# Kernel optimization log

Hardware: AMD Instinct MI355X
Metric: run time of the kernel (lower is better)

## Reference

```python
import jax, jax.numpy as jnp
import numpy as np

B, S, D, H, RANK, NC = 2, 2048, 1024, 16, 128, 16
DH = D // H


def setup_inputs() -> dict:
    key = jax.random.key(0)
    ks = jax.random.split(key, 10)
    x = jax.random.normal(ks[0], (B, S, D), jnp.float32)
    # causal mask, broadcast over batch and heads like torch's [B,1,S,S]
    mask = jnp.tril(jnp.ones((S, S), dtype=bool))[None, None]
    # orthogonal-ish init approximated by scaled gaussian
    compress_neurons = jax.random.normal(ks[1], (NC, D, RANK), jnp.float32) / np.sqrt(D)
    router_Q = jax.random.normal(ks[2], (NC, D), jnp.float32) * 0.02
    router_K = jax.random.normal(ks[3], (NC, D), jnp.float32) * 0.02
    router_V = jax.random.normal(ks[4], (NC, D), jnp.float32) * 0.02
    wQ = jax.random.normal(ks[5], (D, RANK), jnp.float32) / np.sqrt(RANK)
    wK = jax.random.normal(ks[6], (D, RANK), jnp.float32) / np.sqrt(RANK)
    wV = jax.random.normal(ks[7], (D, RANK), jnp.float32) / np.sqrt(RANK)
    wO = jax.random.normal(ks[8], (D, D), jnp.float32) / np.sqrt(D)
    return {"x": x, "mask": mask, "compress_neurons": compress_neurons,
            "router_Q": router_Q, "router_K": router_K, "router_V": router_V,
            "wQ": wQ, "wK": wK, "wV": wV, "wO": wO}


def reference(x, mask, compress_neurons, router_Q, router_K, router_V, wQ, wK, wV, wO):
    def compress(router_w):
        # router scores -> softmax over all n_compress neurons
        w = jax.nn.softmax(jnp.einsum('bsd,nd->bsn', x, router_w), axis=-1)  # [B,S,NC]
        # softmax-weighted sum of all neuron projections (fused einsum)
        return jnp.einsum('bsd,ndr,bsn->bsr', x, compress_neurons, w)  # [B,S,RANK]

    hQ = compress(router_Q)
    hK = compress(router_K)
    hV = compress(router_V)
    # expand rank -> d_model (Linear weight [D,RANK]), then split heads
    Q = jnp.einsum('bsr,dr->bsd', hQ, wQ).reshape(B, S, H, DH).transpose(0, 2, 1, 3)
    K = jnp.einsum('bsr,dr->bsd', hK, wK).reshape(B, S, H, DH).transpose(0, 2, 1, 3)
    V = jnp.einsum('bsr,dr->bsd', hV, wV).reshape(B, S, H, DH).transpose(0, 2, 1, 3)
    scores = jnp.einsum('bhqd,bhkd->bhqk', Q, K) / np.sqrt(DH)  # [B,H,S,S]
    scores = jnp.where(mask, scores, -jnp.inf)
    attn = jax.nn.softmax(scores, axis=-1)
    attn_out = jnp.einsum('bhqk,bhkd->bhqd', attn, V)
    attn_out = attn_out.transpose(0, 2, 1, 3).reshape(B, S, D)
    # dropout omitted (eval mode / dropout=0)
    return jnp.einsum('bsd,ed->bse', attn_out, wO)
```

## Files before the change

### kernel.cpp

```cpp
#include <hip/hip_runtime.h>
#include <hip/hip_bf16.h>
#include <math.h>

#define B_ 2
#define S_ 2048
#define D_ 1024
#define H_ 16
#define RANK_ 128
#define NC_ 16
#define DH_ 64
#define T_ (B_*S_)
#define NZ_ 2176
#define ZW_ 2048

typedef __attribute__((ext_vector_type(8))) __bf16 bf16x8;
typedef __attribute__((ext_vector_type(8))) unsigned short u16x8;
typedef __attribute__((ext_vector_type(4))) unsigned short u16x4;
typedef __attribute__((ext_vector_type(4))) float f32x4;
typedef __attribute__((ext_vector_type(16))) float f32x16;

#if __has_builtin(__builtin_amdgcn_exp2f)
#define EXP2F(x) __builtin_amdgcn_exp2f(x)
#else
#define EXP2F(x) exp2f(x)
#endif

__device__ __forceinline__ unsigned short f2bu(float f) {
    __hip_bfloat16 h = __float2bfloat16(f);
    unsigned short u; __builtin_memcpy(&u, &h, 2); return u;
}
__device__ __forceinline__ float bu2f(unsigned short u) {
    __hip_bfloat16 h; __builtin_memcpy(&h, &u, 2); return __bfloat162float(h);
}

__device__ __forceinline__ void gl_lds16(const unsigned short* g, unsigned short* l) {
    __builtin_amdgcn_global_load_lds(
        (const __attribute__((address_space(1))) void*)g,
        (__attribute__((address_space(3))) void*)l, 16, 0, 0);
}

__device__ __forceinline__ unsigned cvtpk_bf16(float lo, float hi) {
    unsigned r;
    asm("v_cvt_pk_bf16_f32 %0, %1, %2" : "=v"(r) : "v"(lo), "v"(hi));
    return r;
}
__device__ __forceinline__ void plswap(unsigned &a, unsigned &b) {
    asm("v_permlane32_swap_b32 %0, %1" : "+v"(a), "+v"(b));
}

__device__ __forceinline__ bool sniff_f32(const unsigned* __restrict__ p) {
    int votes = 0;
    #pragma unroll
    for (int i = 0; i < 64; i++) {
        unsigned e = (p[i] >> 23) & 0xFFu;
        votes += (e >= 0x60u && e <= 0x8Fu) ? 1 : 0;
    }
    return votes >= 32;
}

struct Cvt { const void* src[9]; unsigned short* dst[9]; const void* C; unsigned short* Ct; };

__global__ __launch_bounds__(256) void k_inputs(Cvt cv,
    const unsigned* __restrict__ probe)
{
    bool f32 = sniff_f32(probe);
    if (blockIdx.x < 512) {
        int bid = blockIdx.x;
        int d0 = (bid & 15) * 64, r0 = ((bid >> 4) & 1) * 64, n = bid >> 5;
        __shared__ unsigned short tile[64][65];
        for (int idx = threadIdx.x; idx < 4096; idx += 256) {
            int row = idx >> 6, col = idx & 63;
            size_t si = ((size_t)n*D_ + d0 + row)*RANK_ + r0 + col;
            tile[row][col] = f32 ? f2bu(((const float*)cv.C)[si])
                                 : ((const unsigned short*)cv.C)[si];
        }
        __syncthreads();
        for (int idx = threadIdx.x; idx < 4096; idx += 256) {
            int row = idx >> 6, col = idx & 63;
            cv.Ct[((size_t)(n*RANK_ + r0 + row))*D_ + d0 + col] = tile[col][row];
        }
        return;
    }
    const int offs[9] = {0, 4194304, 4210688, 4227072, 4243456,
                         4259840, 4390912, 4521984, 4653056};
    const int total4 = 5701632 / 4;
    int nconv = gridDim.x - 512;
    int stride = nconv * 256;
    for (int g = (blockIdx.x - 512) * 256 + threadIdx.x; g < total4; g += stride) {
        int i = g * 4;
        int seg = 0;
        #pragma unroll
        for (int s = 1; s < 9; s++) seg += (i >= offs[s]) ? 1 : 0;
        int local = i - offs[seg];
        const void* sp = cv.src[seg];
        u16x4 v = {0, 0, 0, 0};
        if (sp) {
            if (f32) {
                f32x4 x = *(const f32x4*)((const float*)sp + local);
                #pragma unroll
                for (int j = 0; j < 4; j++) v[j] = f2bu(x[j]);
            } else {
                v = *(const u16x4*)((const unsigned short*)sp + local);
            }
        }
        *(u16x4*)(cv.dst[seg] + local) = v;
    }
}

template<int MT, int MODE>
__global__ __launch_bounds__(256) void k_mfma_gemm(const unsigned short* __restrict__ A,
    const unsigned short* __restrict__ Bm, void* __restrict__ Cout,
    const unsigned* __restrict__ probe, int M, int N, int K)
{
    bool f32out = false;
    if (MODE == 2) f32out = sniff_f32(probe);
    __shared__ __align__(16) unsigned short As[MT*32*32];
    __shared__ __align__(16) unsigned short Bs[128*32];
    const int tid = threadIdx.x;
    const int wv = tid >> 6, lane = tid & 63;
    const int wm = (wv >> 1) * (MT*16), wn = (wv & 1) * 64;
    const int quad = lane >> 4, l16 = lane & 15;
    const int m0 = blockIdx.x * (MT*32), n0 = blockIdx.y * 128;

    const f32x4 z4 = {0.f, 0.f, 0.f, 0.f};
    f32x4 acc[MT][4];
    #pragma unroll
    for (int i = 0; i < MT; i++)
        #pragma unroll
        for (int j = 0; j < 4; j++) acc[i][j] = z4;

    for (int k0 = 0; k0 < K; k0 += 32) {
        __syncthreads();
        #pragma unroll
        for (int c = 0; c < MT/2; c++) {
            int idx = wv*64 + c*256 + lane;
            gl_lds16(A + (size_t)(m0 + (idx >> 2))*K + k0 + (idx & 3)*8,
                     &As[(wv*64 + c*256)*8]);
        }
        #pragma unroll
        for (int c = 0; c < 2; c++) {
            int idx = wv*64 + c*256 + lane;
            gl_lds16(Bm + (size_t)(n0 + (idx >> 2))*K + k0 + (idx & 3)*8,
                     &Bs[(wv*64 + c*256)*8]);
        }
        __syncthreads();
        bf16x8 af[MT], bfr[4];
        #pragma unroll
        for (int mt = 0; mt < MT; mt++) af[mt]  = *(const bf16x8*)&As[(wm + mt*16 + l16)*32 + quad*8];
        #pragma unroll
        for (int nt = 0; nt < 4; nt++) bfr[nt] = *(const bf16x8*)&Bs[(wn + nt*16 + l16)*32 + quad*8];
        #pragma unroll
        for (int mt = 0; mt < MT; mt++)
            #pragma unroll
            for (int nt = 0; nt < 4; nt++)
                acc[mt][nt] = __builtin_amdgcn_mfma_f32_16x16x32_bf16(af[mt], bfr[nt], acc[mt][nt], 0, 0, 0);
    }
    #pragma unroll
    for (int mt = 0; mt < MT; mt++)
        #pragma unroll
        for (int nt = 0; nt < 4; nt++) {
            int col = n0 + wn + nt*16 + l16;
            #pragma unroll
            for (int r = 0; r < 4; r++) {
                int rowg = m0 + wm + mt*16 + quad*4 + r;
                float v = acc[mt][nt][r];
                if (MODE == 2 && f32out) ((float*)Cout)[(size_t)rowg*N + col] = v;
                else  ((unsigned short*)Cout)[(size_t)rowg*N + col] = f2bu(v);
            }
        }
}

__global__ __launch_bounds__(256) void k_zscore(const unsigned short* __restrict__ xc,
    const unsigned short* __restrict__ Ct, unsigned short* __restrict__ z,
    const unsigned short* __restrict__ Rt, float* __restrict__ spart)
{
    __shared__ __align__(16) unsigned short As[128*32];
    __shared__ __align__(16) unsigned short Bs[128*32];
    const int tid = threadIdx.x;
    const int wv = tid >> 6, lane = tid & 63;
    const int quad = lane >> 4, l16 = lane & 15;
    const f32x4 z4 = {0.f, 0.f, 0.f, 0.f};

    if (blockIdx.x < 512) {
        const int wm = (wv >> 1) * 64, wn = (wv & 1) * 64;
        const int m0 = (blockIdx.x & 31) * 128, n0 = (blockIdx.x >> 5) * 128;
        f32x4 acc[4][4];
        #pragma unroll
        for (int i = 0; i < 4; i++)
            #pragma unroll
            for (int j = 0; j < 4; j++) acc[i][j] = z4;

        for (int k0 = 0; k0 < D_; k0 += 32) {
            __syncthreads();
            #pragma unroll
            for (int c = 0; c < 2; c++) {
                int idx = wv*64 + c*256 + lane;
                gl_lds16(xc + (size_t)(m0 + (idx >> 2))*D_ + k0 + (idx & 3)*8,
                         &As[(wv*64 + c*256)*8]);
                gl_lds16(Ct + (size_t)(n0 + (idx >> 2))*D_ + k0 + (idx & 3)*8,
                         &Bs[(wv*64 + c*256)*8]);
            }
            __syncthreads();
            bf16x8 af[4], bfr[4];
            #pragma unroll
            for (int mt = 0; mt < 4; mt++) af[mt]  = *(const bf16x8*)&As[(wm + mt*16 + l16)*32 + quad*8];
            #pragma unroll
            for (int nt = 0; nt < 4; nt++) bfr[nt] = *(const bf16x8*)&Bs[(wn + nt*16 + l16)*32 + quad*8];
            #pragma unroll
            for (int mt = 0; mt < 4; mt++)
                #pragma unroll
                for (int nt = 0; nt < 4; nt++)
                    acc[mt][nt] = __builtin_amdgcn_mfma_f32_16x16x32_bf16(af[mt], bfr[nt], acc[mt][nt], 0, 0, 0);
        }
        #pragma unroll
        for (int mt = 0; mt < 4; mt++)
            #pragma unroll
            for (int nt = 0; nt < 4; nt++) {
                int col = n0 + wn + nt*16 + l16;
                #pragma unroll
                for (int r = 0; r < 4; r++) {
                    int rowg = m0 + wm + mt*16 + quad*4 + r;
                    z[(size_t)rowg*ZW_ + col] = f2bu(acc[mt][nt][r]);
                }
            }
    } else {
        const int id = blockIdx.x - 512;
        const int m0 = (id & 31) * 128;
        const int kc = id >> 5;
        const int wm = wv * 32;
        f32x4 acc[2][4];
        #pragma unroll
        for (int i = 0; i < 2; i++)
            #pragma unroll
            for (int j = 0; j < 4; j++) acc[i][j] = z4;

        for (int k0 = kc*128; k0 < kc*128 + 128; k0 += 32) {
            __syncthreads();
            #pragma unroll
            for (int c = 0; c < 2; c++) {
                int idx = wv*64 + c*256 + lane;
                gl_lds16(xc + (size_t)(m0 + (idx >> 2))*D_ + k0 + (idx & 3)*8,
                         &As[(wv*64 + c*256)*8]);
            }
            {
                int idx = wv*64 + lane;
                gl_lds16(Rt + (size_t)(idx >> 2)*D_ + k0 + (idx & 3)*8,
                         &Bs[(wv*64)*8]);
            }
            __syncthreads();
            bf16x8 af[2], bfr[4];
            #pragma unroll
            for (int mt = 0; mt < 2; mt++) af[mt]  = *(const bf16x8*)&As[(wm + mt*16 + l16)*32 + quad*8];
            #pragma unroll
            for (int nt = 0; nt < 4; nt++) bfr[nt] = *(const bf16x8*)&Bs[(nt*16 + l16)*32 + quad*8];
            #pragma unroll
            for (int mt = 0; mt < 2; mt++)
                #pragma unroll
                for (int nt = 0; nt < 4; nt++)
                    acc[mt][nt] = __builtin_amdgcn_mfma_f32_16x16x32_bf16(af[mt], bfr[nt], acc[mt][nt], 0, 0, 0);
        }
        #pragma unroll
        for (int mt = 0; mt < 2; mt++)
            #pragma unroll
            for (int nt = 0; nt < 4; nt++) {
                int col = nt*16 + l16;
                #pragma unroll
                for (int r = 0; r < 4; r++) {
                    int rowg = m0 + wm + mt*16 + quad*4 + r;
                    spart[(size_t)kc*T_*64 + (size_t)rowg*64 + col] = acc[mt][nt][r];
                }
            }
    }
}

__global__ __launch_bounds__(256) void k_hreduce(const unsigned short* __restrict__ z,
    const float* __restrict__ spart, unsigned short* __restrict__ h)
{
    int t0 = blockIdx.x * 2;
    int tg = threadIdx.x >> 7, r = threadIdx.x & 127;
    int t = t0 + tg;
    __shared__ float sc[2][48];
    __shared__ float wl[2][3][16];
    if (threadIdx.x < 96) {
        int tk = threadIdx.x / 48, j = threadIdx.x % 48;
        float s = 0.f;
        #pragma unroll
        for (int p = 0; p < 8; p++)
            s += spart[(size_t)p*T_*64 + (size_t)(t0 + tk)*64 + j];
        sc[tk][j] = s;
    }
    __syncthreads();
    if (threadIdx.x < 6) {
        int tk = threadIdx.x / 3, w = threadIdx.x % 3;
        float m = -INFINITY;
        for (int n = 0; n < 16; n++) m = fmaxf(m, sc[tk][w*16 + n]);
        float s = 0.f, e[16];
        for (int n = 0; n < 16; n++) { e[n] = __expf(sc[tk][w*16 + n] - m); s += e[n]; }
        float inv = 1.f / s;
        for (int n = 0; n < 16; n++) wl[tk][w][n] = e[n] * inv;
    }
    __syncthreads();
    const unsigned short* zr = z + (size_t)t * ZW_;
    float acc[3] = {0.f, 0.f, 0.f};
    #pragma unroll
    for (int n = 0; n < NC_; n++) {
        float zv = bu2f(zr[n*RANK_ + r]);
        #pragma unroll
        for (int w = 0; w < 3; w++) acc[w] += wl[tg][w][n] * zv;
    }
    #pragma unroll
    for (int w = 0; w < 3; w++) h[((size_t)w*T_ + t)*RANK_ + r] = f2bu(acc[w]);
}

__global__ __launch_bounds__(256) void k_qkv2(const unsigned short* __restrict__ h3,
    const unsigned short* __restrict__ wqkv, unsigned short* __restrict__ QKb,
    unsigned short* __restrict__ Vtg)
{
    __shared__ __align__(16) unsigned short As[128*32];
    __shared__ __align__(16) unsigned short Bs[128*32];
    const int tid = threadIdx.x;
    const int wv = tid >> 6, lane = tid & 63;
    const int wm = (wv >> 1) * 64, wn = (wv & 1) * 64;
    const int quad = lane >> 4, l16 = lane & 15;

    const bool vt = (blockIdx.x >= 512);
    int m0, n0;
    const unsigned short *A, *Bm;
    float scale = 1.f;
    if (!vt) {
        int id = blockIdx.x;
        m0 = (id & 31) * 128;
        n0 = (id >> 5) * 128;
        int w = n0 >> 10;
        A  = h3 + (size_t)w * T_ * RANK_ + (size_t)m0 * RANK_;
        Bm = wqkv + (size_t)w * D_ * RANK_ + (size_t)(n0 & 1023) * RANK_;
        if (w == 0) scale = 0.125f * 1.44269504f;
    } else {
        int id = blockIdx.x - 512;
        m0 = (id & 7) * 128;
        n0 = (id >> 3) * 128;
        A  = wqkv + (size_t)2 * D_ * RANK_ + (size_t)m0 * RANK_;
        Bm = h3 + (size_t)2 * T_ * RANK_ + (size_t)n0 * RANK_;
    }

    const f32x4 z4 = {0.f, 0.f, 0.f, 0.f};
    f32x4 acc[4][4];
    #pragma unroll
    for (int i = 0; i < 4; i++)
        #pragma unroll
        for (int j = 0; j < 4; j++) acc[i][j] = z4;

    for (int k0 = 0; k0 < RANK_; k0 += 32) {
        __syncthreads();
        #pragma unroll
        for (int c = 0; c < 2; c++) {
            int idx = wv*64 + c*256 + lane;
            gl_lds16(A  + (size_t)(idx >> 2)*RANK_ + k0 + (idx & 3)*8,
                     &As[(wv*64 + c*256)*8]);
            gl_lds16(Bm + (size_t)(idx >> 2)*RANK_ + k0 + (idx & 3)*8,
                     &Bs[(wv*64 + c*256)*8]);
        }
        __syncthreads();
        bf16x8 af[4], bfr[4];
        #pragma unroll
        for (int mt = 0; mt < 4; mt++) af[mt]  = *(const bf16x8*)&As[(wm + mt*16 + l16)*32 + quad*8];
        #pragma unroll
        for (int nt = 0; nt < 4; nt++) bfr[nt] = *(const bf16x8*)&Bs[(wn + nt*16 + l16)*32 + quad*8];
        #pragma unroll
        for (int mt = 0; mt < 4; mt++)
            #pragma unroll
            for (int nt = 0; nt < 4; nt++)
                acc[mt][nt] = __builtin_amdgcn_mfma_f32_16x16x32_bf16(af[mt], bfr[nt], acc[mt][nt], 0, 0, 0);
    }
    #pragma unroll
    for (int mt = 0; mt < 4; mt++)
        #pragma unroll
        for (int nt = 0; nt < 4; nt++) {
            #pragma unroll
            for (int r = 0; r < 4; r++) {
                int rowg = m0 + wm + mt*16 + quad*4 + r;
                int col  = n0 + wn + nt*16 + l16;
                float v = acc[mt][nt][r] * scale;
                if (!vt) {
                    QKb[(size_t)(col >> 10)*T_*D_ + (size_t)rowg*D_ + (col & 1023)]
                        = f2bu(v);
                } else {
                    size_t vrow = (size_t)((col >> 11)*H_ + (rowg >> 6))*64 + (rowg & 63);
                    Vtg[vrow*S_ + (col & 2047)] = f2bu(v);
                }
            }
        }
}

__global__ __launch_bounds__(256, 2) void k_flash_mfma(const unsigned short* __restrict__ Qm,
    const unsigned short* __restrict__ Km, const unsigned short* __restrict__ Vtg,
    unsigned short* __restrict__ Om)
{
    const int i = blockIdx.x;
    const int half = i >> 8, r_ = i & 255;
    const int gr = r_ & 31, ts = r_ >> 5;
    const int qt = half ? ts : (15 - ts);
    const int hh = gr & 15, b = gr >> 4;

    __shared__ __align__(16) unsigned short Ks[3][64*64];
    __shared__ __align__(16) unsigned short Vs[3][64*64];
    const int tid = threadIdx.x;
    const int w = tid >> 6, lane = tid & 63;
    const int l32 = lane & 31, hi = lane >> 5;
    const size_t base  = ((size_t)b * S_) * D_ + (size_t)hh * DH_;
    const size_t vbase = (size_t)((b*H_ + hh) * 64) * S_;
    const int tokg = qt*128 + w*32 + l32;

    bf16x8 aq[4];
    #pragma unroll
    for (int ks = 0; ks < 4; ks++)
        aq[ks] = *(const bf16x8*)(Qm + base + (size_t)tokg*D_ + ks*16 + hi*8);

    f32x16 oacc[2];
    #pragma unroll
    for (int db = 0; db < 2; db++)
        #pragma unroll
        for (int ii = 0; ii < 16; ii++) oacc[db][ii] = 0.f;
    float lsum = 0.f;

    const int nkt = 2*(qt + 1);

    auto STAGE = [&](int kt_, int bf_) {
        #pragma unroll
        for (int c = 0; c < 2; c++) {
            int idx = c*256 + tid;
            int row = idx >> 3, j = (idx & 7) ^ (row & 7);
            gl_lds16(Km + base + (size_t)(kt_*64 + row)*D_ + j*8,
                     &Ks[bf_][(c*256 + (w<<6))*8]);
        }
        #pragma unroll
        for (int c = 0; c < 2; c++) {
            int idx = c*256 + tid;
            int row = idx >> 3, j = (idx & 7) ^ (row & 7);
            gl_lds16(Vtg + vbase + (size_t)row*S_ + kt_*64 + j*8,
                     &Vs[bf_][(c*256 + (w<<6))*8]);
        }
    };

    auto QKT = [&](int bf_, f32x16& s0, f32x16& s1) {
        #pragma unroll
        for (int ii = 0; ii < 16; ii++) { s0[ii] = 0.f; s1[ii] = 0.f; }
        const unsigned short* Kp = Ks[bf_];
        #pragma unroll
        for (int ks = 0; ks < 4; ks++) {
            int c0 = (ks*2 + hi) ^ (l32 & 7);
            bf16x8 ak0 = *(const bf16x8*)&Kp[l32*64 + c0*8];
            s0 = __builtin_amdgcn_mfma_f32_32x32x16_bf16(ak0, aq[ks], s0, 0, 0, 0);
            int row1 = 32 + l32;
            int c1 = (ks*2 + hi) ^ (row1 & 7);
            bf16x8 ak1 = *(const bf16x8*)&Kp[row1*64 + c1*8];
            s1 = __builtin_amdgcn_mfma_f32_32x32x16_bf16(ak1, aq[ks], s1, 0, 0, 0);
        }
    };

    STAGE(0, 0);
    STAGE(1, 1);
    __syncthreads();

    f32x16 sA0, sA1, sB0, sB1;
    QKT(0, sA0, sA1);

    for (int kt = 0; kt < nkt; kt++) {
        const int cur = kt % 3;
        if (kt + 2 < nkt) STAGE(kt + 2, (kt + 2) % 3);
        if (kt + 1 < nkt) QKT((kt + 1) % 3, sB0, sB1);

        if (kt >= 2*qt) {
            #pragma unroll
            for (int r = 0; r < 16; r++) {
                int crow = (r&3) + 8*(r>>2) + 4*hi;
                int keyg0 = kt*64 + crow;
                int keyg1 = kt*64 + 32 + crow;
                if (keyg0 > tokg) sA0[r] = -INFINITY;
                if (keyg1 > tokg) sA1[r] = -INFINITY;
            }
        }

        bf16x8 pa[4];
        #pragma unroll
        for (int kb = 0; kb < 2; kb++) {
            float pv[16];
            #pragma unroll
            for (int r = 0; r < 16; r++) {
                pv[r] = EXP2F(kb ? sA1[r] : sA0[r]);
                lsum += pv[r];
            }
            unsigned wd[8];
            #pragma unroll
            for (int j = 0; j < 8; j++) wd[j] = cvtpk_bf16(pv[2*j], pv[2*j+1]);
            plswap(wd[0], wd[2]); plswap(wd[1], wd[3]);
            plswap(wd[4], wd[6]); plswap(wd[5], wd[7]);
            union { unsigned u[4]; bf16x8 v; } u0, u1;
            u0.u[0]=wd[0]; u0.u[1]=wd[1]; u0.u[2]=wd[2]; u0.u[3]=wd[3];
            u1.u[0]=wd[4]; u1.u[1]=wd[5]; u1.u[2]=wd[6]; u1.u[3]=wd[7];
            pa[2*kb]   = u0.v;
            pa[2*kb+1] = u1.v;
        }

        #pragma unroll
        for (int ks = 0; ks < 4; ks++)
            #pragma unroll
            for (int db = 0; db < 2; db++) {
                int row = db*32 + l32;
                int c = (ks*2 + hi) ^ (row & 7);
                bf16x8 bv = *(const bf16x8*)&Vs[cur][row*64 + c*8];
                oacc[db] = __builtin_amdgcn_mfma_f32_32x32x16_bf16(pa[ks], bv, oacc[db], 0, 0, 0);
            }

        if (kt + 1 < nkt) { sA0 = sB0; sA1 = sB1; }
        __syncthreads();
    }

    float l = lsum + __shfl_xor(lsum, 32);
    float inv = 1.f / l;
    #pragma unroll
    for (int r = 0; r < 16; r++) {
        int crow = (r&3) + 8*(r>>2) + 4*hi;
        float invr = __shfl(inv, crow);
        size_t rowo = base + (size_t)(qt*128 + w*32 + crow)*D_;
        #pragma unroll
        for (int db = 0; db < 2; db++)
            Om[rowo + db*32 + l32] = f2bu(oacc[db][r] * invr);
    }
}

extern "C" void kernel_launch(void* const* d_in, const int* in_sizes, int n_in,
                              void* d_out, int out_size, void* d_ws, size_t ws_size,
                              hipStream_t stream)
{
    const unsigned* probe = (const unsigned*)d_in[0];

    unsigned short* u = (unsigned short*)d_ws;
    unsigned short* xc   = u;               size_t o = (size_t)T_*D_;
    unsigned short* wqkv = u + o;           o += (size_t)3*D_*RANK_;
    unsigned short* wOc  = u + o;           o += (size_t)D_*D_;
    unsigned short* Ct   = u + o;           o += (size_t)NZ_*D_;
    unsigned short* h3   = u + o;           o += (size_t)3*T_*RANK_;
    unsigned short* QKb  = u + o;           o += (size_t)2*T_*D_;
    unsigned short* Vtg  = u + o;           o += (size_t)T_*D_;
    unsigned short* z    = u + o;           o += (size_t)T_*NZ_;
    unsigned short* attnb= u + o;           o += (size_t)T_*D_;
    float* spart = (float*)(u + o);         o += (size_t)8*T_*64*2;

    unsigned short* Rp = Ct + (size_t)2048*D_;
    unsigned short* Qb = QKb;
    unsigned short* Kb = QKb + (size_t)T_*D_;

    Cvt cv;
    cv.src[0] = d_in[0]; cv.dst[0] = xc;
    cv.src[1] = d_in[3]; cv.dst[1] = Rp;
    cv.src[2] = d_in[4]; cv.dst[2] = Rp + 16384;
    cv.src[3] = d_in[5]; cv.dst[3] = Rp + 32768;
    cv.src[4] = nullptr; cv.dst[4] = Rp + 49152;
    cv.src[5] = d_in[6]; cv.dst[5] = wqkv;
    cv.src[6] = d_in[7]; cv.dst[6] = wqkv + 131072;
    cv.src[7] = d_in[8]; cv.dst[7] = wqkv + 262144;
    cv.src[8] = d_in[9]; cv.dst[8] = wOc;
    cv.C = d_in[2]; cv.Ct = Ct;
    k_inputs<<<512 + 1024, 256, 0, stream>>>(cv, probe);

    k_zscore<<<768, 256, 0, stream>>>(xc, Ct, z, Rp, spart);

    k_hreduce<<<T_/2, 256, 0, stream>>>(z, spart, h3);

    k_qkv2<<<768, 256, 0, stream>>>(h3, wqkv, QKb, Vtg);

    k_flash_mfma<<<dim3(512), 256, 0, stream>>>(Qb, Kb, Vtg, attnb);

    k_mfma_gemm<2,2><<<dim3(T_/64, D_/128), 256, 0, stream>>>(
        attnb, wOc, d_out, probe, T_, D_, D_);
}
```

Baseline: 208.5 us.

## Split flash attention into 64-query blocks with double buffering

The flash attention kernel now uses 128-thread blocks that each own 64 query rows instead of 256 threads owning 128, giving 1024 blocks with a four-slot interleaved ordering of causal tile lengths for load balance. The triple-buffered K/V pipeline with QK^T computed one tile ahead is replaced by a simpler double buffer where QK^T is computed in the same iteration. The aim is more, smaller blocks for better CU occupancy and tail balance, and less LDS per block. The cost is less software overlap of QK^T with softmax and PV, plus more total K/V tile loads across blocks.

After: 217.3 us. 4.2% more time.

```diff
diff --git a/kernel.cpp b/kernel.cpp
--- a/kernel.cpp
+++ b/kernel.cpp
@@ -392,24 +392,28 @@
         }
 }
 
-__global__ __launch_bounds__(256, 2) void k_flash_mfma(const unsigned short* __restrict__ Qm,
+__global__ __launch_bounds__(128) void k_flash_mfma(const unsigned short* __restrict__ Qm,
     const unsigned short* __restrict__ Km, const unsigned short* __restrict__ Vtg,
     unsigned short* __restrict__ Om)
 {
-    const int i = blockIdx.x;
-    const int half = i >> 8, r_ = i & 255;
-    const int gr = r_ & 31, ts = r_ >> 5;
-    const int qt = half ? ts : (15 - ts);
+    const int x = blockIdx.x;
+    const int slot = x >> 8, rr = x & 255;
+    const int ts = rr >> 5, gr = rr & 31;
+    int qt;
+    if      (slot == 0) qt = 31 - ts;
+    else if (slot == 1) qt = ts;
+    else if (slot == 2) qt = 23 - ts;
+    else                qt = 8 + ts;
     const int hh = gr & 15, b = gr >> 4;
 
-    __shared__ __align__(16) unsigned short Ks[3][64*64];
-    __shared__ __align__(16) unsigned short Vs[3][64*64];
+    __shared__ __align__(16) unsigned short Ks[2][64*64];
+    __shared__ __align__(16) unsigned short Vs[2][64*64];
     const int tid = threadIdx.x;
     const int w = tid >> 6, lane = tid & 63;
     const int l32 = lane & 31, hi = lane >> 5;
     const size_t base  = ((size_t)b * S_) * D_ + (size_t)hh * DH_;
     const size_t vbase = (size_t)((b*H_ + hh) * 64) * S_;
-    const int tokg = qt*128 + w*32 + l32;
+    const int tokg = qt*64 + w*32 + l32;
 
     bf16x8 aq[4];
     #pragma unroll
@@ -423,62 +427,56 @@
         for (int ii = 0; ii < 16; ii++) oacc[db][ii] = 0.f;
     float lsum = 0.f;
 
-    const int nkt = 2*(qt + 1);
+    const int nkt = qt + 1;
 
     auto STAGE = [&](int kt_, int bf_) {
         #pragma unroll
-        for (int c = 0; c < 2; c++) {
-            int idx = c*256 + tid;
+        for (int c = 0; c < 4; c++) {
+            int idx = c*128 + tid;
             int row = idx >> 3, j = (idx & 7) ^ (row & 7);
             gl_lds16(Km + base + (size_t)(kt_*64 + row)*D_ + j*8,
-                     &Ks[bf_][(c*256 + (w<<6))*8]);
-        }
-        #pragma unroll
-        for (int c = 0; c < 2; c++) {
-            int idx = c*256 + tid;
+                     &Ks[bf_][(c*128 + (w<<6))*8]);
+        }
+        #pragma unroll
+        for (int c = 0; c < 4; c++) {
+            int idx = c*128 + tid;
             int row = idx >> 3, j = (idx & 7) ^ (row & 7);
             gl_lds16(Vtg + vbase + (size_t)row*S_ + kt_*64 + j*8,
-                     &Vs[bf_][(c*256 + (w<<6))*8]);
+                     &Vs[bf_][(c*128 + (w<<6))*8]);
         }
     };
 
-    auto QKT = [&](int bf_, f32x16& s0, f32x16& s1) {
-        #pragma unroll
-        for (int ii = 0; ii < 16; ii++) { s0[ii] = 0.f; s1[ii] = 0.f; }
-        const unsigned short* Kp = Ks[bf_];
-        #pragma unroll
-        for (int ks = 0; ks < 4; ks++) {
-            int c0 = (ks*2 + hi) ^ (l32 & 7);
-            bf16x8 ak0 = *(const bf16x8*)&Kp[l32*64 + c0*8];
-            s0 = __builtin_amdgcn_mfma_f32_32x32x16_bf16(ak0, aq[ks], s0, 0, 0, 0);
-            int row1 = 32 + l32;
-            int c1 = (ks*2 + hi) ^ (row1 & 7);
-            bf16x8 ak1 = *(const bf16x8*)&Kp[row1*64 + c1*8];
-            s1 = __builtin_amdgcn_mfma_f32_32x32x16_bf16(ak1, aq[ks], s1, 0, 0, 0);
-        }
-    };
-
     STAGE(0, 0);
-    STAGE(1, 1);
-    __syncthreads();
-
-    f32x16 sA0, sA1, sB0, sB1;
-    QKT(0, sA0, sA1);
 
     for (int kt = 0; kt < nkt; kt++) {
-        const int cur = kt % 3;
-        if (kt + 2 < nkt) STAGE(kt + 2, (kt + 2) % 3);
-        if (kt + 1 < nkt) QKT((kt + 1) % 3, sB0, sB1);
-
-        if (kt >= 2*qt) {
-            #pragma unroll
-            for (int r = 0; r < 16; r++) {
-                int crow = (r&3) + 8*(r>>2) + 4*hi;
-                int keyg0 = kt*64 + crow;
-                int keyg1 = kt*64 + 32 + crow;
-                if (keyg0 > tokg) sA0[r] = -INFINITY;
-                if (keyg1 > tokg) sA1[r] = -INFINITY;
-            }
+        const int cur = kt & 1;
+        __syncthreads();
+
+        if (kt + 1 < nkt) STAGE(kt + 1, 1 - cur);
+
+        f32x16 sacc[2];
+        #pragma unroll
+        for (int kb = 0; kb < 2; kb++)
+            #pragma unroll
+            for (int ii = 0; ii < 16; ii++) sacc[kb][ii] = 0.f;
+        #pragma unroll
+        for (int ks = 0; ks < 4; ks++)
+            #pragma unroll
+            for (int kb = 0; kb < 2; kb++) {
+                int row = kb*32 + l32;
+                int c = (ks*2 + hi) ^ (row & 7);
+                bf16x8 ak = *(const bf16x8*)&Ks[cur][row*64 + c*8];
+                sacc[kb] = __builtin_amdgcn_mfma_f32_32x32x16_bf16(ak, aq[ks], sacc[kb], 0, 0, 0);
+            }
+
+        if (kt == qt) {
+            #pragma unroll
+            for (int kb = 0; kb < 2; kb++)
+                #pragma unroll
+                for (int r = 0; r < 16; r++) {
+                    int keyg = kt*64 + kb*32 + (r&3) + 8*(r>>2) + 4*hi;
+                    if (keyg > tokg) sacc[kb][r] = -INFINITY;
+                }
         }
 
         bf16x8 pa[4];
@@ -487,7 +485,7 @@
             float pv[16];
             #pragma unroll
             for (int r = 0; r < 16; r++) {
-                pv[r] = EXP2F(kb ? sA1[r] : sA0[r]);
+                pv[r] = EXP2F(sacc[kb][r]);
                 lsum += pv[r];
             }
             unsigned wd[8];
@@ -511,9 +509,6 @@
                 bf16x8 bv = *(const bf16x8*)&Vs[cur][row*64 + c*8];
                 oacc[db] = __builtin_amdgcn_mfma_f32_32x32x16_bf16(pa[ks], bv, oacc[db], 0, 0, 0);
             }
-
-        if (kt + 1 < nkt) { sA0 = sB0; sA1 = sB1; }
-        __syncthreads();
     }
 
     float l = lsum + __shfl_xor(lsum, 32);
@@ -522,7 +517,7 @@
     for (int r = 0; r < 16; r++) {
         int crow = (r&3) + 8*(r>>2) + 4*hi;
         float invr = __shfl(inv, crow);
-        size_t rowo = base + (size_t)(qt*128 + w*32 + crow)*D_;
+        size_t rowo = base + (size_t)(qt*64 + w*32 + crow)*D_;
         #pragma unroll
         for (int db = 0; db < 2; db++)
             Om[rowo + db*32 + l32] = f2bu(oacc[db][r] * invr);
@@ -570,7 +565,7 @@
 
     k_qkv2<<<768, 256, 0, stream>>>(h3, wqkv, QKb, Vtg);
 
-    k_flash_mfma<<<dim3(512), 256, 0, stream>>>(Qb, Kb, Vtg, attnb);
+    k_flash_mfma<<<dim3(1024), 128, 0, stream>>>(Qb, Kb, Vtg, attnb);
 
     k_mfma_gemm<2,2><<<dim3(T_/64, D_/128), 256, 0, stream>>>(
         attnb, wOc, d_out, probe, T_, D_, D_);
```
